# Optimization experiments

Measured on AMD Instinct MI355X. Metric: run time of the kernel, lower is better.

Reference implementation:

```python
import jax, jax.numpy as jnp
import numpy as np

DIM = 256  # channel width
B, H, W = 4, 64, 64


def conv2d(x, w, b, pad, groups=1):
    # x: NCHW, w: OIHW (I = C_in/groups)
    y = jax.lax.conv_general_dilated(
        x, w, window_strides=(1, 1),
        padding=[(pad[0], pad[0]), (pad[1], pad[1])],
        dimension_numbers=("NCHW", "OIHW", "NCHW"),
        feature_group_count=groups)
    return y + b[None, :, None, None]


def l2norm(x, eps=1e-12):
    # matches F.normalize(x, dim=-1): x / max(||x||_2, eps)
    n = jnp.sqrt(jnp.sum(x * x, axis=-1, keepdims=True))
    return x / jnp.maximum(n, eps)


def setup_inputs() -> dict:
    key = jax.random.key(0)
    ks = jax.random.split(key, 12)
    dim, c8 = DIM, DIM // 8
    w = lambda k, shape, s: jax.random.normal(k, shape, jnp.float32) * s
    return {
        "x": jax.random.normal(ks[0], (B, dim, H, W), jnp.float32),
        "w_conv": w(ks[1], (dim, dim, 3, 3), 0.02), "b_conv": jnp.zeros((dim,), jnp.float32),
        "w01": w(ks[2], (dim, 1, 1, 7), 0.05), "b01": jnp.zeros((dim,), jnp.float32),
        "w02": w(ks[3], (dim, 1, 7, 1), 0.05), "b02": jnp.zeros((dim,), jnp.float32),
        "w11": w(ks[4], (dim, 1, 1, 11), 0.05), "b11": jnp.zeros((dim,), jnp.float32),
        "w12": w(ks[5], (dim, 1, 11, 1), 0.05), "b12": jnp.zeros((dim,), jnp.float32),
        "w21": w(ks[6], (dim, 1, 1, 21), 0.05), "b21": jnp.zeros((dim,), jnp.float32),
        "w22": w(ks[7], (dim, 1, 21, 1), 0.05), "b22": jnp.zeros((dim,), jnp.float32),
        "w_proj": w(ks[8], (c8, dim, 1, 1), 0.05), "b_proj": jnp.zeros((c8,), jnp.float32),
        "w3": w(ks[9], (c8, dim // 4, 1, 1), 0.05), "b3": jnp.zeros((c8,), jnp.float32),
        "w4": w(ks[10], (dim, c8, 1, 1), 0.05), "b4": jnp.zeros((dim,), jnp.float32),
    }


def reference(x, w_conv, b_conv, w01, b01, w02, b02, w11, b11, w12, b12,
              w21, b21, w22, b22, w_proj, b_proj, w3, b3, w4, b4):
    b, c, h, w_ = x.shape
    x = conv2d(x, w_conv, b_conv, (1, 1))
    # multi-scale separable depthwise convs (7, 11, 21)
    x1 = conv2d(conv2d(x, w01, b01, (0, 3), c), w02, b02, (3, 0), c)
    x2 = conv2d(conv2d(x, w11, b11, (0, 5), c), w12, b12, (5, 0), c)
    x3 = conv2d(conv2d(x, w21, b21, (0, 10), c), w22, b22, (10, 0), c)
    out1 = x1 + x2 + x3 + x                      # [b, dim, h, w]
    out1 = conv2d(out1, w_proj, b_proj, (0, 0))  # [b, dim//8, h, w]
    c8 = out1.shape[1]
    t = out1.reshape(b, c8, h * w_)              # b head c (h w), head=1

    q1 = l2norm(t)
    attn1 = jax.nn.softmax(q1 @ jnp.swapaxes(q1, -2, -1), axis=-1)  # [b, c8, c8]
    out2 = attn1 @ t                                                # [b, c8, hw]

    # branch 2: spatial attention (hw x hw)
    ts = jnp.swapaxes(t, -2, -1)                 # [b, hw, c8]
    q2 = l2norm(ts)
    attn2 = jax.nn.softmax(q2 @ jnp.swapaxes(q2, -2, -1), axis=-1)  # [b, hw, hw]
    out3 = jnp.swapaxes(attn2 @ ts, -2, -1)                         # [b, c8, hw]

    out4 = jnp.concatenate([out2.reshape(b, c8, h, w_),
                            out3.reshape(b, c8, h, w_)], axis=1)    # [b, dim//4, h, w]
    out5 = conv2d(out4, w3, b3, (0, 0)) + out1
    return conv2d(out5, w4, b4, (0, 0))          # [b, dim, h, w]
```

## Files before the change

kernel.cpp:

```cpp
#include <hip/hip_runtime.h>
#include <hip/hip_bf16.h>

typedef __hip_bfloat16 bf16;
typedef short s16;
typedef __attribute__((ext_vector_type(4))) short s16x4;
typedef __attribute__((ext_vector_type(8))) short s16x8;
typedef __attribute__((ext_vector_type(4))) float f32x4;

__device__ __forceinline__ s16 f2b(float f){
    unsigned u = __float_as_uint(f);
    unsigned r = (u + 0x7FFFu + ((u >> 16) & 1u)) >> 16;
    return (s16)r;
}
__device__ __forceinline__ float b2f_bits(s16 v){
    return __uint_as_float(((unsigned)(unsigned short)v) << 16);
}

__global__ __launch_bounds__(256) void xtrans_k(const float* __restrict__ x, s16* __restrict__ xcl){
    __shared__ s16 lb[64][258];
    int h = blockIdx.x, b = blockIdx.y, t = threadIdx.x;
    for (int i = t; i < 16384; i += 256){
        int ci = i >> 6, w = i & 63;
        lb[w][ci] = f2b(x[((b*256 + ci)*64 + h)*64 + w]);
    }
    __syncthreads();
    for (int i = t; i < 16384; i += 256){
        int w = i >> 8, ci = i & 255;
        xcl[(b*4096 + h*64 + w)*256 + ci] = lb[w][ci];
    }
}

__global__ __launch_bounds__(256) void wpack_k(const float* __restrict__ w, s16* __restrict__ wpk){
    int idx = blockIdx.x*256 + threadIdx.x;
    int cil = idx & 31;
    int r   = idx >> 5;
    int co  = r & 255;
    int r2  = r >> 8;
    int tap = r2 % 9, cc = r2 / 9;
    wpk[idx] = f2b(w[(co*256 + cc*32 + cil)*9 + tap]);
}

__global__ __launch_bounds__(256) void conv3x3m_k(const s16* __restrict__ xcl,
        const s16* __restrict__ wpk, const float* __restrict__ bias,
        bf16* __restrict__ y0){
    __shared__ alignas(16) s16 smem[30240];
    s16* xls = smem;
    s16* wls = smem + 9504;
    const int sp = blockIdx.x, cog = blockIdx.y;
    const int b = sp >> 5, h0 = (sp & 31)*2;
    const int t = threadIdx.x;
    const int wv = t >> 6, lane = t & 63;
    const int lm = lane & 15, g = lane >> 4;

    f32x4 acc[2][4];
    #pragma unroll
    for (int mi = 0; mi < 2; ++mi)
        #pragma unroll
        for (int ni = 0; ni < 4; ++ni) acc[mi][ni] = (f32x4){0.f,0.f,0.f,0.f};

    for (int cc = 0; cc < 8; ++cc){
        __syncthreads();
        for (int i = t; i < 1056; i += 256){
            int g8 = i & 3, wi = (i>>2) % 66, r = (i>>2) / 66;
            int h = h0 - 1 + r, w = wi - 1;
            s16x8 v = {0,0,0,0,0,0,0,0};
            if (h >= 0 && h < 64 && w >= 0 && w < 64)
                v = *(const s16x8*)&xcl[(b*4096 + h*64 + w)*256 + cc*32 + g8*8];
            s16* d = &xls[(r*66 + wi)*36 + g8*8];
            *(s16x4*)d       = __builtin_shufflevector(v, v, 0,1,2,3);
            *(s16x4*)(d + 4) = __builtin_shufflevector(v, v, 4,5,6,7);
        }
        for (int i = t; i < 2304; i += 256){
            int g8 = i & 3, co = (i>>2) & 63, tap = i >> 8;
            s16x8 v = *(const s16x8*)&wpk[((cc*9 + tap)*256 + cog*64 + co)*32 + g8*8];
            s16* d = &wls[(tap*64 + co)*36 + g8*8];
            *(s16x4*)d       = __builtin_shufflevector(v, v, 0,1,2,3);
            *(s16x4*)(d + 4) = __builtin_shufflevector(v, v, 4,5,6,7);
        }
        __syncthreads();
        #pragma unroll
        for (int tap = 0; tap < 9; ++tap){
            const int kh = tap/3, kw = tap%3;
            s16x8 bfr[4], afr[2];
            #pragma unroll
            for (int ni = 0; ni < 4; ++ni){
                const s16* p = &wls[(tap*64 + ni*16 + lm)*36 + g*8];
                s16x4 lo = *(const s16x4*)p;
                s16x4 hi = *(const s16x4*)(p + 4);
                bfr[ni] = __builtin_shufflevector(lo, hi, 0,1,2,3,4,5,6,7);
            }
            #pragma unroll
            for (int mi = 0; mi < 2; ++mi){
                int m = (wv*2 + mi)*16 + lm;
                int hr = m >> 6, ww = m & 63;
                const s16* p = &xls[((hr + kh)*66 + (ww + kw))*36 + g*8];
                s16x4 lo = *(const s16x4*)p;
                s16x4 hi = *(const s16x4*)(p + 4);
                afr[mi] = __builtin_shufflevector(lo, hi, 0,1,2,3,4,5,6,7);
            }
            #pragma unroll
            for (int mi = 0; mi < 2; ++mi)
                #pragma unroll
                for (int ni = 0; ni < 4; ++ni)
                    acc[mi][ni] = __builtin_amdgcn_mfma_f32_16x16x32_bf16(
                        afr[mi], bfr[ni], acc[mi][ni], 0, 0, 0);
        }
    }
    __syncthreads();
    float* ot = (float*)smem;
    #pragma unroll
    for (int mi = 0; mi < 2; ++mi)
        #pragma unroll
        for (int ni = 0; ni < 4; ++ni)
            #pragma unroll
            for (int r = 0; r < 4; ++r){
                int m  = (wv*2 + mi)*16 + g*4 + r;
                int co = ni*16 + lm;
                ot[co*132 + m] = acc[mi][ni][r];
            }
    __syncthreads();
    for (int i = t; i < 8192; i += 256){
        int co = i >> 7, m = i & 127;
        float v = ot[co*132 + m] + bias[cog*64 + co];
        y0[((b*256 + cog*64 + co)*64 + h0 + (m>>6))*64 + (m & 63)] = __float2bfloat16(v);
    }
}

template<int K>
__device__ __forceinline__ void sep_branch(const float (*__restrict__ pl)[65], float (*__restrict__ hp)[65],
                                           int c, int t,
                                           const float* __restrict__ wh, const float* __restrict__ bh,
                                           const float* __restrict__ wv, const float* __restrict__ bv,
                                           float* acc){
    constexpr int P = K/2;
    constexpr int W = 16 + 2*P;
    float wk[K];
    #pragma unroll
    for (int j = 0; j < K; ++j) wk[j] = wh[c*K + j];
    float bhv = bh[c];
    {
        int h = t >> 2, w0 = (t & 3)*16;
        float win[W];
        #pragma unroll
        for (int j = 0; j < W; ++j){
            int ww = w0 - P + j;
            win[j] = (ww >= 0 && ww < 64) ? pl[h][ww] : 0.f;
        }
        __syncthreads();
        #pragma unroll
        for (int i = 0; i < 16; ++i){
            float s = bhv;
            #pragma unroll
            for (int k = 0; k < K; ++k) s += win[i+k]*wk[k];
            hp[h][w0 + i] = s;
        }
    }
    float vk[K];
    #pragma unroll
    for (int j = 0; j < K; ++j) vk[j] = wv[c*K + j];
    float bvv = bv[c];
    __syncthreads();
    {
        int w = t & 63, h0 = (t >> 6)*16;
        float win[W];
        #pragma unroll
        for (int j = 0; j < W; ++j){
            int hh = h0 - P + j;
            win[j] = (hh >= 0 && hh < 64) ? hp[hh][w] : 0.f;
        }
        #pragma unroll
        for (int i = 0; i < 16; ++i){
            float s = bvv;
            #pragma unroll
            for (int k = 0; k < K; ++k) s += win[i+k]*vk[k];
            acc[i] += s;
        }
    }
}

__global__ __launch_bounds__(256) void sepconv_k(const bf16* __restrict__ y0,
        const float* __restrict__ w01, const float* __restrict__ b01,
        const float* __restrict__ w02, const float* __restrict__ b02,
        const float* __restrict__ w11, const float* __restrict__ b11,
        const float* __restrict__ w12, const float* __restrict__ b12,
        const float* __restrict__ w21, const float* __restrict__ b21,
        const float* __restrict__ w22, const float* __restrict__ b22,
        bf16* __restrict__ out1){
    __shared__ float pl[64][65];
    __shared__ float hp[64][65];
    int bc = blockIdx.x;
    int c = bc & 255;
    int t = threadIdx.x;
    const bf16* src = y0 + bc*4096;
    for (int i = t; i < 4096; i += 256) pl[i>>6][i&63] = __bfloat162float(src[i]);
    __syncthreads();
    float acc[16];
    #pragma unroll
    for (int k = 0; k < 16; ++k) acc[k] = 0.f;
    sep_branch<7 >(pl, hp, c, t, w01, b01, w02, b02, acc);
    sep_branch<11>(pl, hp, c, t, w11, b11, w12, b12, acc);
    sep_branch<21>(pl, hp, c, t, w21, b21, w22, b22, acc);
    bf16* dst = out1 + bc*4096;
    {
        int w = t & 63, h0 = (t >> 6)*16;
        #pragma unroll
        for (int i = 0; i < 16; ++i)
            dst[(h0 + i)*64 + w] = __float2bfloat16(acc[i] + pl[h0 + i][w]);
    }
}

__global__ __launch_bounds__(256) void proj_k(const bf16* __restrict__ out1, const float* __restrict__ wp,
                                              const float* __restrict__ bp, float* __restrict__ tbuf,
                                              s16* __restrict__ tTb, float* __restrict__ rn2){
    __shared__ float wl[256*32];
    __shared__ s16 part[4][64][36];
    int pt = blockIdx.x, b = blockIdx.y, t = threadIdx.x;
    int q = t >> 6, lane = t & 63;
    for (int i = t; i < 8192; i += 256){
        int ci = i >> 5, cc = i & 31;
        wl[ci*32 + cc] = wp[cc*256 + ci];
    }
    __syncthreads();
    int p = pt*64 + lane;
    float acc[32] = {};
    const bf16* xb = out1 + b*1048576 + p;
    for (int ci = q*64; ci < q*64 + 64; ++ci){
        float v = __bfloat162float(xb[ci*4096]);
        const float* wr = &wl[ci*32];
        #pragma unroll
        for (int c8 = 0; c8 < 8; ++c8){
            float4 w4 = *(const float4*)&wr[c8*4];
            acc[c8*4+0] += w4.x*v; acc[c8*4+1] += w4.y*v;
            acc[c8*4+2] += w4.z*v; acc[c8*4+3] += w4.w*v;
        }
    }
    #pragma unroll
    for (int cc = 0; cc < 32; ++cc) part[q][lane][cc] = f2b(acc[cc]);
    __syncthreads();
    int p_loc = t >> 2, qq = t & 3;
    int pg = pt*64 + p_loc;
    float a8[8];
    float ss = 0.f;
    #pragma unroll
    for (int c = 0; c < 8; ++c){
        int cc = qq*8 + c;
        float v = b2f_bits(part[0][p_loc][cc]) + b2f_bits(part[1][p_loc][cc])
                + b2f_bits(part[2][p_loc][cc]) + b2f_bits(part[3][p_loc][cc]) + bp[cc];
        a8[c] = v;
        ss += v*v;
    }
    ss += __shfl_xor(ss, 1, 4);
    ss += __shfl_xor(ss, 2, 4);
    if (qq == 0) rn2[b*4096 + pg] = 1.f / fmaxf(sqrtf(ss), 1e-12f);
    #pragma unroll
    for (int c = 0; c < 8; ++c) tbuf[(b*32 + qq*8 + c)*4096 + pg] = a8[c];
    s16x8 o8;
    #pragma unroll
    for (int c = 0; c < 8; ++c) o8[c] = f2b(a8[c]);
    *(s16x8*)&tTb[(b*4096 + pg)*32 + qq*8] = o8;
}

__global__ __launch_bounds__(256) void rn1_k(const float* __restrict__ tbuf, float* __restrict__ rn1){
    int row = blockIdx.x;
    int t = threadIdx.x;
    float ss = 0.f;
    const float* r = tbuf + row*4096;
    for (int p = t; p < 4096; p += 256){ float v = r[p]; ss += v*v; }
    #pragma unroll
    for (int o = 32; o > 0; o >>= 1) ss += __shfl_down(ss, o, 64);
    __shared__ float red[4];
    if ((t & 63) == 0) red[t >> 6] = ss;
    __syncthreads();
    if (t == 0){
        float tot = red[0]+red[1]+red[2]+red[3];
        rn1[row] = 1.f / fmaxf(sqrtf(tot), 1e-12f);
    }
}

__global__ __launch_bounds__(256) void gram2_k(const float* __restrict__ tbuf, float* __restrict__ part){
    __shared__ float tl[128][33];
    int ps = blockIdx.x, b = blockIdx.y, t = threadIdx.x;
    for (int idx = t; idx < 4096; idx += 256){
        int cc = idx >> 7, pp = idx & 127;
        tl[pp][cc] = tbuf[(b*32+cc)*4096 + ps*128 + pp];
    }
    __syncthreads();
    #pragma unroll
    for (int k = 0; k < 4; ++k){
        int pair = k*256 + t;
        int i = pair >> 5, j = pair & 31;
        float s = 0.f;
        #pragma unroll 4
        for (int pp = 0; pp < 128; ++pp) s += tl[pp][i]*tl[pp][j];
        part[(b*32+ps)*1024 + pair] = s;
    }
}

__global__ __launch_bounds__(64) void attn1_k(const float* __restrict__ part, const float* __restrict__ rn1,
                                              float* __restrict__ attn1T){
    int i = blockIdx.x, b = blockIdx.y, j = threadIdx.x;
    float e = 0.f;
    if (j < 32){
        float g = 0.f;
        #pragma unroll 8
        for (int ps = 0; ps < 32; ++ps) g += part[(b*32+ps)*1024 + i*32 + j];
        e = __expf(rn1[b*32+i]*rn1[b*32+j]*g);
    }
    float sum = e;
    #pragma unroll
    for (int o = 32; o > 0; o >>= 1) sum += __shfl_xor(sum, o, 64);
    if (j < 32) attn1T[b*1024 + j*32 + i] = e / sum;
}

__global__ __launch_bounds__(256) void out2_k(const float* __restrict__ tbuf, const float* __restrict__ attn1T,
                                              float* __restrict__ out2){
    __shared__ float al[1024];
    int pt = blockIdx.x, b = blockIdx.y, t = threadIdx.x;
    for (int i = t; i < 1024; i += 256) al[i] = attn1T[b*1024 + i];
    __syncthreads();
    int p = pt*256 + t;
    float acc[32] = {};
    for (int j = 0; j < 32; ++j){
        float tv = tbuf[(b*32+j)*4096 + p];
        #pragma unroll
        for (int q = 0; q < 8; ++q){
            float4 a = *(const float4*)&al[j*32 + q*4];
            acc[q*4+0] += a.x*tv; acc[q*4+1] += a.y*tv; acc[q*4+2] += a.z*tv; acc[q*4+3] += a.w*tv;
        }
    }
    #pragma unroll
    for (int i = 0; i < 32; ++i) out2[(b*32+i)*4096 + p] = acc[i];
}

__global__ __launch_bounds__(256) void flashm_k(const s16* __restrict__ tTb, const float* __restrict__ rn2,
                                                float* __restrict__ partA, float* __restrict__ partL){
    __shared__ alignas(16) s16 kvb[128*36];
    __shared__ alignas(16) s16 vts[32*132];
    __shared__ alignas(16) s16 pls[4][16*132];
    __shared__ float rnj[128];
    __shared__ float ri[64];
    const int ib = blockIdx.x, b = blockIdx.y, chunk = blockIdx.z;
    const int t = threadIdx.x, wv = t >> 6, lane = t & 63;
    const int lm = lane & 15, g = lane >> 4;
    const int i0 = ib*64;

    if (t < 64) ri[t] = rn2[b*4096 + i0 + t];
    s16x8 qf = *(const s16x8*)&tTb[(b*4096 + i0 + wv*16 + lm)*32 + g*8];
    __syncthreads();
    float rni4[4];
    #pragma unroll
    for (int r = 0; r < 4; ++r) rni4[r] = ri[wv*16 + g*4 + r];

    f32x4 oacc[2];
    oacc[0] = (f32x4){0.f,0.f,0.f,0.f};
    oacc[1] = (f32x4){0.f,0.f,0.f,0.f};
    float lacc[4] = {0.f,0.f,0.f,0.f};
    s16* pw = pls[wv];

    for (int jt = chunk*16; jt < chunk*16 + 16; ++jt){
        const int j0 = jt*128;
        __syncthreads();
        for (int gi = t; gi < 512; gi += 256){
            int j = gi >> 2, g8 = gi & 3;
            s16x8 v = *(const s16x8*)&tTb[(b*4096 + j0 + j)*32 + g8*8];
            s16* d = &kvb[j*36 + g8*8];
            *(s16x4*)d       = __builtin_shufflevector(v, v, 0,1,2,3);
            *(s16x4*)(d + 4) = __builtin_shufflevector(v, v, 4,5,6,7);
            #pragma unroll
            for (int e = 0; e < 8; ++e) vts[(g8*8 + e)*132 + j] = v[e];
        }
        if (t < 128) rnj[t] = rn2[b*4096 + j0 + t];
        __syncthreads();
        #pragma unroll
        for (int nt = 0; nt < 8; ++nt){
            const s16* bp = &kvb[(nt*16 + lm)*36 + g*8];
            s16x4 blo = *(const s16x4*)bp;
            s16x4 bhi = *(const s16x4*)(bp + 4);
            s16x8 bf = __builtin_shufflevector(blo, bhi, 0,1,2,3,4,5,6,7);
            f32x4 s = __builtin_amdgcn_mfma_f32_16x16x32_bf16(qf, bf,
                        (f32x4){0.f,0.f,0.f,0.f}, 0, 0, 0);
            float rj = rnj[nt*16 + lm];
            #pragma unroll
            for (int r = 0; r < 4; ++r){
                float e = __expf(s[r]*rni4[r]*rj);
                lacc[r] += e;
                pw[(g*4 + r)*132 + nt*16 + lm] = f2b(e);
            }
        }
        #pragma unroll
        for (int ks = 0; ks < 4; ++ks){
            const s16* ap = &pw[lm*132 + ks*32 + g*8];
            s16x4 alo = *(const s16x4*)ap;
            s16x4 ahi = *(const s16x4*)(ap + 4);
            s16x8 af = __builtin_shufflevector(alo, ahi, 0,1,2,3,4,5,6,7);
            #pragma unroll
            for (int n2 = 0; n2 < 2; ++n2){
                const s16* vp = &vts[(n2*16 + lm)*132 + ks*32 + g*8];
                s16x4 vlo = *(const s16x4*)vp;
                s16x4 vhi = *(const s16x4*)(vp + 4);
                s16x8 vf = __builtin_shufflevector(vlo, vhi, 0,1,2,3,4,5,6,7);
                oacc[n2] = __builtin_amdgcn_mfma_f32_16x16x32_bf16(af, vf, oacc[n2], 0, 0, 0);
            }
        }
    }
    #pragma unroll
    for (int r = 0; r < 4; ++r){
        float v = lacc[r];
        v += __shfl_xor(v, 1, 16); v += __shfl_xor(v, 2, 16);
        v += __shfl_xor(v, 4, 16); v += __shfl_xor(v, 8, 16);
        lacc[r] = v;
    }
    const int base = (b*2 + chunk)*4096 + i0 + wv*16;
    #pragma unroll
    for (int n2 = 0; n2 < 2; ++n2)
        #pragma unroll
        for (int r = 0; r < 4; ++r)
            partA[(base + g*4 + r)*32 + n2*16 + lm] = oacc[n2][r];
    if (lm == 0){
        #pragma unroll
        for (int r = 0; r < 4; ++r) partL[base + g*4 + r] = lacc[r];
    }
}

__global__ __launch_bounds__(256) void mrg2_k(const float* __restrict__ partA, const float* __restrict__ partL,
                                              float* __restrict__ out3T){
    int it = blockIdx.x, b = blockIdx.y, t = threadIdx.x;
    int r = t >> 2, g = t & 3;
    int i = it*64 + r;
    float l = partL[(b*2 + 0)*4096 + i] + partL[(b*2 + 1)*4096 + i];
    float inv = 1.f / l;
    float o[8];
    #pragma unroll
    for (int k = 0; k < 8; ++k)
        o[k] = partA[((b*2 + 0)*4096 + i)*32 + g*8 + k] + partA[((b*2 + 1)*4096 + i)*32 + g*8 + k];
    float* op = out3T + (b*4096 + i)*32 + g*8;
    #pragma unroll
    for (int k = 0; k < 8; ++k) op[k] = o[k]*inv;
}

__global__ __launch_bounds__(256) void out5_k(const float* __restrict__ out2, const float* __restrict__ out3T,
                                              const float* __restrict__ tbuf, const float* __restrict__ w3,
                                              const float* __restrict__ b3, float* __restrict__ out5){
    __shared__ float w3T[64*32];
    int pt = blockIdx.x, b = blockIdx.y, t = threadIdx.x;
    for (int i = t; i < 2048; i += 256){
        int j = i >> 5, cc = i & 31;
        w3T[i] = w3[cc*64 + j];
    }
    __syncthreads();
    int p = pt*256 + t;
    float acc[32];
    #pragma unroll
    for (int cc = 0; cc < 32; ++cc) acc[cc] = b3[cc] + tbuf[(b*32+cc)*4096 + p];
    for (int j = 0; j < 32; ++j){
        float v = out2[(b*32+j)*4096 + p];
        #pragma unroll
        for (int q = 0; q < 8; ++q){
            float4 a = *(const float4*)&w3T[j*32 + q*4];
            acc[q*4] += a.x*v; acc[q*4+1] += a.y*v; acc[q*4+2] += a.z*v; acc[q*4+3] += a.w*v;
        }
    }
    const float* o3 = out3T + (b*4096 + p)*32;
    float v3[32];
    #pragma unroll
    for (int q = 0; q < 8; ++q){
        float4 v = *(const float4*)&o3[q*4];
        v3[q*4]=v.x; v3[q*4+1]=v.y; v3[q*4+2]=v.z; v3[q*4+3]=v.w;
    }
    #pragma unroll
    for (int j = 0; j < 32; ++j){
        float v = v3[j];
        #pragma unroll
        for (int q = 0; q < 8; ++q){
            float4 a = *(const float4*)&w3T[(32+j)*32 + q*4];
            acc[q*4] += a.x*v; acc[q*4+1] += a.y*v; acc[q*4+2] += a.z*v; acc[q*4+3] += a.w*v;
        }
    }
    #pragma unroll
    for (int cc = 0; cc < 32; ++cc) out5[(b*32+cc)*4096 + p] = acc[cc];
}

__global__ __launch_bounds__(256) void final_k(const float* __restrict__ out5, const float* __restrict__ w4,
                                               const float* __restrict__ b4, float* __restrict__ out){
    __shared__ float w4T[32*64];
    int pt = blockIdx.x, cog = blockIdx.y, b = blockIdx.z, t = threadIdx.x;
    for (int i = t; i < 2048; i += 256){
        int cc = i >> 6, co = i & 63;
        w4T[i] = w4[(cog*64+co)*32 + cc];
    }
    __syncthreads();
    int p = pt*256 + t;
    float acc[64];
    #pragma unroll
    for (int co = 0; co < 64; ++co) acc[co] = b4[cog*64+co];
    for (int cc = 0; cc < 32; ++cc){
        float v = out5[(b*32+cc)*4096 + p];
        #pragma unroll
        for (int q = 0; q < 16; ++q){
            float4 a = *(const float4*)&w4T[cc*64 + q*4];
            acc[q*4] += a.x*v; acc[q*4+1] += a.y*v; acc[q*4+2] += a.z*v; acc[q*4+3] += a.w*v;
        }
    }
    #pragma unroll
    for (int co = 0; co < 64; ++co)
        out[(b*256 + cog*64 + co)*4096 + p] = acc[co];
}

extern "C" void kernel_launch(void* const* d_in, const int* in_sizes, int n_in,
                              void* d_out, int out_size, void* d_ws, size_t ws_size,
                              hipStream_t stream) {
    const float* x      = (const float*)d_in[0];
    const float* w_conv = (const float*)d_in[1];
    const float* b_conv = (const float*)d_in[2];
    const float* w01 = (const float*)d_in[3];  const float* b01 = (const float*)d_in[4];
    const float* w02 = (const float*)d_in[5];  const float* b02 = (const float*)d_in[6];
    const float* w11 = (const float*)d_in[7];  const float* b11 = (const float*)d_in[8];
    const float* w12 = (const float*)d_in[9];  const float* b12 = (const float*)d_in[10];
    const float* w21 = (const float*)d_in[11]; const float* b21 = (const float*)d_in[12];
    const float* w22 = (const float*)d_in[13]; const float* b22 = (const float*)d_in[14];
    const float* w_proj = (const float*)d_in[15]; const float* b_proj = (const float*)d_in[16];
    const float* w3 = (const float*)d_in[17]; const float* b3 = (const float*)d_in[18];
    const float* w4 = (const float*)d_in[19]; const float* b4 = (const float*)d_in[20];

    char* wsb = (char*)d_ws;
    s16*   xcl  = (s16*)wsb;
    bf16*  out1 = (bf16*)wsb;
    bf16*  y0   = (bf16*)(wsb + 8388608);
    s16*   wpk  = (s16*)(wsb + 16777216);
    float* f    = (float*)d_ws;
    float* part   = f + 0;
    float* partA  = f + 0;
    float* tbuf   = f + 2097152;
    s16*   tTb    = (s16*)(wsb + 10485760);
    float* out2   = f + 3145728;
    float* out3T  = f + 3670016;
    float* out5   = f + 4194304;
    float* partL  = f + 4194304;
    float* rn1    = f + 4718592;
    float* attn1T = f + 4722816;
    float* rn2    = f + 4726912;

    xtrans_k<<<dim3(64, 4), 256, 0, stream>>>(x, xcl);
    wpack_k<<<dim3(2304), 256, 0, stream>>>(w_conv, wpk);
    conv3x3m_k<<<dim3(128, 4), 256, 0, stream>>>(xcl, wpk, b_conv, y0);
    sepconv_k<<<dim3(1024), 256, 0, stream>>>(y0, w01, b01, w02, b02,
                                              w11, b11, w12, b12,
                                              w21, b21, w22, b22, out1);
    proj_k<<<dim3(64, 4), 256, 0, stream>>>(out1, w_proj, b_proj, tbuf, tTb, rn2);
    rn1_k<<<dim3(128), 256, 0, stream>>>(tbuf, rn1);
    gram2_k<<<dim3(32, 4), 256, 0, stream>>>(tbuf, part);
    attn1_k<<<dim3(32, 4), 64, 0, stream>>>(part, rn1, attn1T);
    out2_k<<<dim3(16, 4), 256, 0, stream>>>(tbuf, attn1T, out2);
    flashm_k<<<dim3(64, 4, 2), 256, 0, stream>>>(tTb, rn2, partA, partL);
    mrg2_k<<<dim3(64, 4), 256, 0, stream>>>(partA, partL, out3T);
    out5_k<<<dim3(16, 4), 256, 0, stream>>>(out2, out3T, tbuf, w3, b3, out5);
    final_k<<<dim3(16, 4, 4), 256, 0, stream>>>(out5, w4, b4, (float*)d_out);
}
```

Baseline: 335.3 us.

## Fold channel-attention and 1x1 convs into per-batch weights, fuse tail kernels

The linear tail (attn1 @ t, w3 conv, residual, w4 conv) is folded algebraically into per-batch 256x32 matrices, computed by a small fold kernel. One fused final kernel then merges the flash partials and applies those matrices directly to t and out3. rn1 is taken from the Gram matrix diagonal, which removes the rn1 and out2 kernels and their intermediate buffers. The cost is extra FLOPs per output (64 MACs per output channel instead of 32) and a serial single-block fold kernel per batch.

```diff
diff --git a/kernel.cpp b/kernel.cpp
--- a/kernel.cpp
+++ b/kernel.cpp
@@ -260,23 +260,6 @@
     *(s16x8*)&tTb[(b*4096 + pg)*32 + qq*8] = o8;
 }
 
-__global__ __launch_bounds__(256) void rn1_k(const float* __restrict__ tbuf, float* __restrict__ rn1){
-    int row = blockIdx.x;
-    int t = threadIdx.x;
-    float ss = 0.f;
-    const float* r = tbuf + row*4096;
-    for (int p = t; p < 4096; p += 256){ float v = r[p]; ss += v*v; }
-    #pragma unroll
-    for (int o = 32; o > 0; o >>= 1) ss += __shfl_down(ss, o, 64);
-    __shared__ float red[4];
-    if ((t & 63) == 0) red[t >> 6] = ss;
-    __syncthreads();
-    if (t == 0){
-        float tot = red[0]+red[1]+red[2]+red[3];
-        rn1[row] = 1.f / fmaxf(sqrtf(tot), 1e-12f);
-    }
-}
-
 __global__ __launch_bounds__(256) void gram2_k(const float* __restrict__ tbuf, float* __restrict__ part){
     __shared__ float tl[128][33];
     int ps = blockIdx.x, b = blockIdx.y, t = threadIdx.x;
@@ -296,40 +279,68 @@
     }
 }
 
-__global__ __launch_bounds__(64) void attn1_k(const float* __restrict__ part, const float* __restrict__ rn1,
+__global__ __launch_bounds__(64) void attn1_k(const float* __restrict__ part,
                                               float* __restrict__ attn1T){
     int i = blockIdx.x, b = blockIdx.y, j = threadIdx.x;
-    float e = 0.f;
+    float gij = 0.f, gjj = 0.f;
     if (j < 32){
-        float g = 0.f;
         #pragma unroll 8
-        for (int ps = 0; ps < 32; ++ps) g += part[(b*32+ps)*1024 + i*32 + j];
-        e = __expf(rn1[b*32+i]*rn1[b*32+j]*g);
-    }
+        for (int ps = 0; ps < 32; ++ps){
+            const float* pp = part + (b*32+ps)*1024;
+            gij += pp[i*32 + j];
+            gjj += pp[j*33];
+        }
+    }
+    float rnj = 1.f / fmaxf(sqrtf(gjj), 1e-12f);
+    float rni = __shfl(rnj, i, 64);
+    float e = (j < 32) ? __expf(rni*rnj*gij) : 0.f;
     float sum = e;
     #pragma unroll
     for (int o = 32; o > 0; o >>= 1) sum += __shfl_xor(sum, o, 64);
     if (j < 32) attn1T[b*1024 + j*32 + i] = e / sum;
 }
 
-__global__ __launch_bounds__(256) void out2_k(const float* __restrict__ tbuf, const float* __restrict__ attn1T,
-                                              float* __restrict__ out2){
-    __shared__ float al[1024];
-    int pt = blockIdx.x, b = blockIdx.y, t = threadIdx.x;
-    for (int i = t; i < 1024; i += 256) al[i] = attn1T[b*1024 + i];
-    __syncthreads();
-    int p = pt*256 + t;
-    float acc[32] = {};
+__global__ __launch_bounds__(256) void fold_k(const float* __restrict__ attn1T,
+        const float* __restrict__ w3, const float* __restrict__ b3,
+        const float* __restrict__ w4, const float* __restrict__ b4,
+        float* __restrict__ WtT, float* __restrict__ WoT, float* __restrict__ bfo){
+    __shared__ float a1[1024];
+    __shared__ float w3a[1024];
+    __shared__ float w3bs[1024];
+    int b = blockIdx.x, t = threadIdx.x;
+    for (int idx = t; idx < 1024; idx += 256){
+        int i = idx >> 5, j = idx & 31;
+        a1[idx]   = attn1T[b*1024 + j*32 + i];
+        w3bs[idx] = w3[i*64 + 32 + j];
+    }
+    __syncthreads();
+    for (int idx = t; idx < 1024; idx += 256){
+        int cc = idx >> 5, j = idx & 31;
+        float s = 0.f;
+        #pragma unroll 8
+        for (int i = 0; i < 32; ++i) s += w3[cc*64 + i]*a1[i*32 + j];
+        w3a[idx] = s;
+    }
+    __syncthreads();
+    int co = t;
+    float w4r[32];
+    #pragma unroll
+    for (int cc = 0; cc < 32; ++cc) w4r[cc] = w4[co*32 + cc];
+    float bfv = b4[co];
+    #pragma unroll
+    for (int cc = 0; cc < 32; ++cc) bfv += w4r[cc]*b3[cc];
+    bfo[b*256 + co] = bfv;
     for (int j = 0; j < 32; ++j){
-        float tv = tbuf[(b*32+j)*4096 + p];
-        #pragma unroll
-        for (int q = 0; q < 8; ++q){
-            float4 a = *(const float4*)&al[j*32 + q*4];
-            acc[q*4+0] += a.x*tv; acc[q*4+1] += a.y*tv; acc[q*4+2] += a.z*tv; acc[q*4+3] += a.w*tv;
-        }
-    }
-    #pragma unroll
-    for (int i = 0; i < 32; ++i) out2[(b*32+i)*4096 + p] = acc[i];
+        float st = w4r[j];
+        float so = 0.f;
+        #pragma unroll 8
+        for (int cc = 0; cc < 32; ++cc){
+            st += w4r[cc]*w3a[cc*32 + j];
+            so += w4r[cc]*w3bs[cc*32 + j];
+        }
+        WtT[(b*32 + j)*256 + co] = st;
+        WoT[(b*32 + j)*256 + co] = so;
+    }
 }
 
 __global__ __launch_bounds__(256) void flashm_k(const s16* __restrict__ tTb, const float* __restrict__ rn2,
@@ -422,88 +433,38 @@
     }
 }
 
-__global__ __launch_bounds__(256) void mrg2_k(const float* __restrict__ partA, const float* __restrict__ partL,
-                                              float* __restrict__ out3T){
-    int it = blockIdx.x, b = blockIdx.y, t = threadIdx.x;
-    int r = t >> 2, g = t & 3;
-    int i = it*64 + r;
-    float l = partL[(b*2 + 0)*4096 + i] + partL[(b*2 + 1)*4096 + i];
+__global__ __launch_bounds__(256) void finalfuse_k(const float* __restrict__ tbuf,
+        const float* __restrict__ partA, const float* __restrict__ partL,
+        const float* __restrict__ WtT, const float* __restrict__ WoT,
+        const float* __restrict__ bfo, float* __restrict__ out){
+    int pt = blockIdx.x, cog = blockIdx.y, b = blockIdx.z, t = threadIdx.x;
+    int p = pt*256 + t;
+    float l = partL[(b*2 + 0)*4096 + p] + partL[(b*2 + 1)*4096 + p];
     float inv = 1.f / l;
-    float o[8];
-    #pragma unroll
-    for (int k = 0; k < 8; ++k)
-        o[k] = partA[((b*2 + 0)*4096 + i)*32 + g*8 + k] + partA[((b*2 + 1)*4096 + i)*32 + g*8 + k];
-    float* op = out3T + (b*4096 + i)*32 + g*8;
-    #pragma unroll
-    for (int k = 0; k < 8; ++k) op[k] = o[k]*inv;
-}
-
-__global__ __launch_bounds__(256) void out5_k(const float* __restrict__ out2, const float* __restrict__ out3T,
-                                              const float* __restrict__ tbuf, const float* __restrict__ w3,
-                                              const float* __restrict__ b3, float* __restrict__ out5){
-    __shared__ float w3T[64*32];
-    int pt = blockIdx.x, b = blockIdx.y, t = threadIdx.x;
-    for (int i = t; i < 2048; i += 256){
-        int j = i >> 5, cc = i & 31;
-        w3T[i] = w3[cc*64 + j];
-    }
-    __syncthreads();
-    int p = pt*256 + t;
+    const float* pa0 = partA + ((b*2 + 0)*4096 + p)*32;
+    const float* pa1 = partA + ((b*2 + 1)*4096 + p)*32;
+    float v3[32];
+    #pragma unroll
+    for (int q = 0; q < 8; ++q){
+        float4 a = *(const float4*)&pa0[q*4];
+        float4 c = *(const float4*)&pa1[q*4];
+        v3[q*4+0] = (a.x + c.x)*inv; v3[q*4+1] = (a.y + c.y)*inv;
+        v3[q*4+2] = (a.z + c.z)*inv; v3[q*4+3] = (a.w + c.w)*inv;
+    }
     float acc[32];
     #pragma unroll
-    for (int cc = 0; cc < 32; ++cc) acc[cc] = b3[cc] + tbuf[(b*32+cc)*4096 + p];
+    for (int co = 0; co < 32; ++co) acc[co] = bfo[b*256 + cog*32 + co];
     for (int j = 0; j < 32; ++j){
-        float v = out2[(b*32+j)*4096 + p];
-        #pragma unroll
-        for (int q = 0; q < 8; ++q){
-            float4 a = *(const float4*)&w3T[j*32 + q*4];
-            acc[q*4] += a.x*v; acc[q*4+1] += a.y*v; acc[q*4+2] += a.z*v; acc[q*4+3] += a.w*v;
-        }
-    }
-    const float* o3 = out3T + (b*4096 + p)*32;
-    float v3[32];
-    #pragma unroll
-    for (int q = 0; q < 8; ++q){
-        float4 v = *(const float4*)&o3[q*4];
-        v3[q*4]=v.x; v3[q*4+1]=v.y; v3[q*4+2]=v.z; v3[q*4+3]=v.w;
-    }
-    #pragma unroll
-    for (int j = 0; j < 32; ++j){
-        float v = v3[j];
-        #pragma unroll
-        for (int q = 0; q < 8; ++q){
-            float4 a = *(const float4*)&w3T[(32+j)*32 + q*4];
-            acc[q*4] += a.x*v; acc[q*4+1] += a.y*v; acc[q*4+2] += a.z*v; acc[q*4+3] += a.w*v;
-        }
-    }
-    #pragma unroll
-    for (int cc = 0; cc < 32; ++cc) out5[(b*32+cc)*4096 + p] = acc[cc];
-}
-
-__global__ __launch_bounds__(256) void final_k(const float* __restrict__ out5, const float* __restrict__ w4,
-                                               const float* __restrict__ b4, float* __restrict__ out){
-    __shared__ float w4T[32*64];
-    int pt = blockIdx.x, cog = blockIdx.y, b = blockIdx.z, t = threadIdx.x;
-    for (int i = t; i < 2048; i += 256){
-        int cc = i >> 6, co = i & 63;
-        w4T[i] = w4[(cog*64+co)*32 + cc];
-    }
-    __syncthreads();
-    int p = pt*256 + t;
-    float acc[64];
-    #pragma unroll
-    for (int co = 0; co < 64; ++co) acc[co] = b4[cog*64+co];
-    for (int cc = 0; cc < 32; ++cc){
-        float v = out5[(b*32+cc)*4096 + p];
-        #pragma unroll
-        for (int q = 0; q < 16; ++q){
-            float4 a = *(const float4*)&w4T[cc*64 + q*4];
-            acc[q*4] += a.x*v; acc[q*4+1] += a.y*v; acc[q*4+2] += a.z*v; acc[q*4+3] += a.w*v;
-        }
-    }
-    #pragma unroll
-    for (int co = 0; co < 64; ++co)
-        out[(b*256 + cog*64 + co)*4096 + p] = acc[co];
+        float vt = tbuf[(b*32 + j)*4096 + p];
+        float vo = v3[j];
+        const float* wtr = WtT + (b*32 + j)*256 + cog*32;
+        const float* wor = WoT + (b*32 + j)*256 + cog*32;
+        #pragma unroll
+        for (int co = 0; co < 32; ++co) acc[co] += wtr[co]*vt + wor[co]*vo;
+    }
+    #pragma unroll
+    for (int co = 0; co < 32; ++co)
+        out[((b*256 + cog*32 + co)*4096) + p] = acc[co];
 }
 
 extern "C" void kernel_launch(void* const* d_in, const int* in_sizes, int n_in,
@@ -532,11 +493,10 @@
     float* partA  = f + 0;
     float* tbuf   = f + 2097152;
     s16*   tTb    = (s16*)(wsb + 10485760);
-    float* out2   = f + 3145728;
-    float* out3T  = f + 3670016;
-    float* out5   = f + 4194304;
+    float* WtT    = f + 3145728;
+    float* WoT    = f + 3178496;
+    float* bfo    = f + 3211264;
     float* partL  = f + 4194304;
-    float* rn1    = f + 4718592;
     float* attn1T = f + 4722816;
     float* rn2    = f + 4726912;
 
@@ -547,12 +507,10 @@
                                               w11, b11, w12, b12,
                                               w21, b21, w22, b22, out1);
     proj_k<<<dim3(64, 4), 256, 0, stream>>>(out1, w_proj, b_proj, tbuf, tTb, rn2);
-    rn1_k<<<dim3(128), 256, 0, stream>>>(tbuf, rn1);
     gram2_k<<<dim3(32, 4), 256, 0, stream>>>(tbuf, part);
-    attn1_k<<<dim3(32, 4), 64, 0, stream>>>(part, rn1, attn1T);
-    out2_k<<<dim3(16, 4), 256, 0, stream>>>(tbuf, attn1T, out2);
+    attn1_k<<<dim3(32, 4), 64, 0, stream>>>(part, attn1T);
+    fold_k<<<dim3(4), 256, 0, stream>>>(attn1T, w3, b3, w4, b4, WtT, WoT, bfo);
     flashm_k<<<dim3(64, 4, 2), 256, 0, stream>>>(tTb, rn2, partA, partL);
-    mrg2_k<<<dim3(64, 4), 256, 0, stream>>>(partA, partL, out3T);
-    out5_k<<<dim3(16, 4), 256, 0, stream>>>(out2, out3T, tbuf, w3, b3, out5);
-    final_k<<<dim3(16, 4, 4), 256, 0, stream>>>(out5, w4, b4, (float*)d_out);
-}
+    finalfuse_k<<<dim3(16, 8, 4), 256, 0, stream>>>(tbuf, partA, partL, WtT, WoT, bfo,
+                                                    (float*)d_out);
+}
```

Result: faster. 323.8 us (-3.4%).
